# Kernel optimization log

Hardware: AMD Instinct MI355X
Metric: run time of the kernel (lower is better)

The kernel has to match this reference:

```python
import jax, jax.numpy as jnp
import numpy as np

H = 256  # hidden_dim


def _bidir_lstm_layer(x, W_ih, W_hh, bias):
    """x: [S, B, in]; W_ih: [2, in, 4H]; W_hh: [2, H, 4H]; bias: [2, 4H].
    Returns [S, B, 2H] (forward || backward outputs per timestep).
    PyTorch gate order: i, f, g, o."""
    B = x.shape[1]
    init = (jnp.zeros((B, H), x.dtype), jnp.zeros((B, H), x.dtype))
    # precompute input projections for the whole sequence, both directions
    xp = jnp.einsum('sbi,dij->dsbj', x, W_ih) + bias[:, None, None, :]  # [2,S,B,4H]

    def make_step(W_hh_d):
        def step(carry, xt):
            h, c = carry
            g = xt + h @ W_hh_d  # [B, 4H]
            i = jax.nn.sigmoid(g[:, :H])
            f = jax.nn.sigmoid(g[:, H:2 * H])
            gg = jnp.tanh(g[:, 2 * H:3 * H])
            o = jax.nn.sigmoid(g[:, 3 * H:])
            c = f * c + i * gg
            h = o * jnp.tanh(c)
            return (h, c), h
        return step

    _, h_f = jax.lax.scan(make_step(W_hh[0]), init, xp[0])
    _, h_b = jax.lax.scan(make_step(W_hh[1]), init, xp[1], reverse=True)
    return jnp.concatenate([h_f, h_b], axis=-1)  # [S, B, 2H]


def setup_inputs() -> dict:
    key = jax.random.key(0)
    ks = jax.random.split(key, 11)
    s = 0.05  # small init scale to keep gates in their dynamic range
    inp = {
        'x': jax.random.normal(ks[0], (8192, 1024), jnp.float32),
        'w_ih0': jax.random.normal(ks[1], (2, 1024, 4 * H), jnp.float32) * s,
        'w_hh0': jax.random.normal(ks[2], (2, H, 4 * H), jnp.float32) * s,
        'b0': jax.random.normal(ks[3], (2, 4 * H), jnp.float32) * s,
        'w_ih': jax.random.normal(ks[4], (4, 2, 2 * H, 4 * H), jnp.float32) * s,
        'w_hh': jax.random.normal(ks[5], (4, 2, H, 4 * H), jnp.float32) * s,
        'b': jax.random.normal(ks[6], (4, 2, 4 * H), jnp.float32) * s,
        'w1': jax.random.normal(ks[7], (2 * H, 32), jnp.float32) * s,
        'b1': jax.random.normal(ks[8], (32,), jnp.float32) * s,
        'w2': jax.random.normal(ks[9], (32, 2), jnp.float32) * s,
        'b2': jax.random.normal(ks[10], (2,), jnp.float32) * s,
    }
    return inp


def reference(x, w_ih0, w_hh0, b0, w_ih, w_hh, b, w1, b1, w2, b2):
    # x: [S, 1024] -> [S, B=1, 1024] (module does unsqueeze(0).transpose(0,1))
    h = x[:, None, :]
    h = _bidir_lstm_layer(h, w_ih0, w_hh0, b0)
    for l in range(4):  # layers 1..4 (fixed count)
        h = _bidir_lstm_layer(h, w_ih[l], w_hh[l], b[l])
    # cat(forward output at last step, backward output at first step)
    feat = jnp.concatenate([h[-1, :, :H], h[0, :, H:]], axis=1)  # [1, 2H]
    out = (feat @ w1 + b1) @ w2 + b2  # [1, 2]
    return out
```

## Files before the change

kernel.cpp:

```cpp
#include <hip/hip_runtime.h>

constexpr int SQ = 8192;
constexpr int HD = 256;
constexpr int NG = 1024;

typedef __fp16 h2 __attribute__((ext_vector_type(2)));
typedef unsigned int uint;
typedef unsigned short ushort;

__device__ __forceinline__ float sigm_f(float x) {
  float e = __builtin_amdgcn_exp2f(-1.4426950408889634f * x);
  return __builtin_amdgcn_rcpf(1.0f + e);
}
__device__ __forceinline__ float tanh_f(float x) {
  float e = __builtin_amdgcn_exp2f(2.885390081777927f * x);
  return 1.0f - 2.0f * __builtin_amdgcn_rcpf(1.0f + e);
}
__device__ __forceinline__ h2 bch2(uint v) { return __builtin_bit_cast(h2, v); }
__device__ __forceinline__ uint pk(float a, float b) {
  return __builtin_bit_cast(uint, __builtin_amdgcn_cvt_pkrtz(a, b));
}
__device__ __forceinline__ float dpp_xor1(float x) {
  int v = __builtin_amdgcn_mov_dpp(__builtin_bit_cast(int, x), 0xB1, 0xF, 0xF, true);
  return __builtin_bit_cast(float, v);
}

__global__ __launch_bounds__(256) void gemm_xp(const float* __restrict__ A, int K,
                                               const float* __restrict__ W,
                                               const float* __restrict__ bias,
                                               float* __restrict__ out) {
  __shared__ float Al[16][64];
  __shared__ float Bl[16][64];
  const int tid = threadIdx.x;
  const int bm = blockIdx.x * 64;
  const int d  = blockIdx.y >> 4;
  const int bn = (blockIdx.y & 15) * 64;
  const float* Wd = W + (size_t)d * K * NG;
  const float* bd = bias + (size_t)d * NG;
  float* outd = out + (size_t)d * SQ * NG;

  const int m4 = (tid >> 4) << 2;
  const int n4 = (tid & 15) << 2;
  const int am = tid >> 2, ak = (tid & 3) << 2;
  const int bk = tid >> 4, bnn = (tid & 15) << 2;

  float acc[4][4] = {};
  for (int kt = 0; kt < K; kt += 16) {
    float4 av = *(const float4*)(A + (size_t)(bm + am) * K + kt + ak);
    float4 bv = *(const float4*)(Wd + (size_t)(kt + bk) * NG + bn + bnn);
    __syncthreads();
    Al[ak + 0][am] = av.x;
    Al[ak + 1][am] = av.y;
    Al[ak + 2][am] = av.z;
    Al[ak + 3][am] = av.w;
    *(float4*)&Bl[bk][bnn] = bv;
    __syncthreads();
#pragma unroll
    for (int k = 0; k < 16; ++k) {
      float4 a = *(const float4*)&Al[k][m4];
      float4 b = *(const float4*)&Bl[k][n4];
      float ar[4] = {a.x, a.y, a.z, a.w};
      float br[4] = {b.x, b.y, b.z, b.w};
#pragma unroll
      for (int i = 0; i < 4; ++i)
#pragma unroll
        for (int jj = 0; jj < 4; ++jj)
          acc[i][jj] = fmaf(ar[i], br[jj], acc[i][jj]);
    }
  }
#pragma unroll
  for (int i = 0; i < 4; ++i) {
    float4 o;
    o.x = acc[i][0] + bd[bn + n4 + 0];
    o.y = acc[i][1] + bd[bn + n4 + 1];
    o.z = acc[i][2] + bd[bn + n4 + 2];
    o.w = acc[i][3] + bd[bn + n4 + 3];
    *(float4*)(outd + (size_t)(bm + m4 + i) * NG + bn + n4) = o;
  }
}

__global__ __launch_bounds__(512, 1) void lstm_rec11(const float* __restrict__ Whh,
                                                     const float* __restrict__ xp,
                                                     float* __restrict__ obuf) {
  __shared__ uint4 wl[16 * 512];
  __shared__ uint  hl[2][128];
  const int d = blockIdx.x;
  const int j = threadIdx.x;
  const int u = j >> 1;
  const int s = j & 1;
  const float* W   = Whh + (size_t)d * HD * NG;
  const float* xpd = xp + (size_t)d * SQ * NG;

  for (int idx = j; idx < 16 * 512; idx += 512) {
    const int rem = idx & 511;
    const int uu  = rem >> 1;
    const int ss  = rem & 1;
    const int qq  = (idx >> 9) & 3;
    const int g   = idx >> 11;
    const int r0  = ss * 128 + 96 + 8 * qq;
    const int c   = g * 256 + uu;
    uint4 v;
    v.x = pk(W[(size_t)(r0 + 0) * NG + c], W[(size_t)(r0 + 1) * NG + c]);
    v.y = pk(W[(size_t)(r0 + 2) * NG + c], W[(size_t)(r0 + 3) * NG + c]);
    v.z = pk(W[(size_t)(r0 + 4) * NG + c], W[(size_t)(r0 + 5) * NG + c]);
    v.w = pk(W[(size_t)(r0 + 6) * NG + c], W[(size_t)(r0 + 7) * NG + c]);
    wl[idx] = v;
  }

  h2 wr[4][48];
#pragma unroll
  for (int g = 0; g < 4; ++g) {
    const float* Wc = W + (size_t)(s * 128) * NG + g * 256 + u;
#pragma unroll
    for (int k = 0; k < 48; ++k)
      wr[g][k] = __builtin_amdgcn_cvt_pkrtz(Wc[(size_t)(2 * k) * NG],
                                            Wc[(size_t)(2 * k + 1) * NG]);
  }

  if (j < 256) { ((uint*)hl)[j] = 0u; }
  __syncthreads();

  const int fwd = (d == 0) ? 1 : 0;
  int t = fwd ? 0 : SQ - 1;
  const int dt = fwd ? 1 : -1;
  float cc = 0.0f;
  int p = 0;

  float xc[4], xn[4] = {};
#pragma unroll
  for (int g = 0; g < 4; ++g) xc[g] = xpd[(size_t)t * NG + g * 256 + u];

  for (int step = 0; step < SQ; ++step) {
    if (step + 1 < SQ) {
#pragma unroll
      for (int g = 0; g < 4; ++g) xn[g] = xpd[(size_t)(t + dt) * NG + g * 256 + u];
    }

    const uint4* hb = (const uint4*)&hl[p][s * 64];
    float acc[4] = {0.0f, 0.0f, 0.0f, 0.0f};
#pragma unroll
    for (int q = 0; q < 12; ++q) {
      uint4 hq = hb[q];
      h2 hx = bch2(hq.x), hy = bch2(hq.y), hz = bch2(hq.z), hw = bch2(hq.w);
#pragma unroll
      for (int g = 0; g < 4; ++g) {
        acc[g] = __builtin_amdgcn_fdot2(wr[g][4 * q + 0], hx, acc[g], false);
        acc[g] = __builtin_amdgcn_fdot2(wr[g][4 * q + 1], hy, acc[g], false);
        acc[g] = __builtin_amdgcn_fdot2(wr[g][4 * q + 2], hz, acc[g], false);
        acc[g] = __builtin_amdgcn_fdot2(wr[g][4 * q + 3], hw, acc[g], false);
      }
    }
#pragma unroll
    for (int qq = 0; qq < 4; ++qq) {
      uint4 hq = hb[12 + qq];
      h2 hx = bch2(hq.x), hy = bch2(hq.y), hz = bch2(hq.z), hw = bch2(hq.w);
#pragma unroll
      for (int g = 0; g < 4; ++g) {
        uint4 wq = wl[(g * 4 + qq) * 512 + j];
        acc[g] = __builtin_amdgcn_fdot2(bch2(wq.x), hx, acc[g], false);
        acc[g] = __builtin_amdgcn_fdot2(bch2(wq.y), hy, acc[g], false);
        acc[g] = __builtin_amdgcn_fdot2(bch2(wq.z), hz, acc[g], false);
        acc[g] = __builtin_amdgcn_fdot2(bch2(wq.w), hw, acc[g], false);
      }
    }

#pragma unroll
    for (int g = 0; g < 4; ++g) acc[g] += dpp_xor1(acc[g]);

    float iv = sigm_f(acc[0] + xc[0]);
    float fv = sigm_f(acc[1] + xc[1]);
    float gv = tanh_f(acc[2] + xc[2]);
    float ov = sigm_f(acc[3] + xc[3]);
    cc = fv * cc + iv * gv;
    float hv = ov * tanh_f(cc);

    if (s == 0) {
      obuf[(size_t)t * 512 + (d << 8) + u] = hv;
      ((ushort*)hl[p ^ 1])[u] = (ushort)(pk(hv, hv) & 0xFFFFu);
    }

    asm volatile("s_waitcnt lgkmcnt(0)" ::: "memory");
    __builtin_amdgcn_s_barrier();
    __builtin_amdgcn_sched_barrier(0);

    p ^= 1;
#pragma unroll
    for (int g = 0; g < 4; ++g) xc[g] = xn[g];
    t += dt;
  }
}

__global__ void cls_k(const float* __restrict__ buf, const float* __restrict__ w1,
                      const float* __restrict__ b1, const float* __restrict__ w2,
                      const float* __restrict__ b2, float* __restrict__ out) {
  __shared__ float feat[512];
  __shared__ float hid[32];
  const int t = threadIdx.x;
  feat[t] = (t < 256) ? buf[(size_t)(SQ - 1) * 512 + t] : buf[t];
  __syncthreads();
  if (t < 32) {
    float a = b1[t];
    for (int k = 0; k < 512; ++k) a = fmaf(feat[k], w1[k * 32 + t], a);
    hid[t] = a;
  }
  __syncthreads();
  if (t < 2) {
    float a = b2[t];
    for (int k = 0; k < 32; ++k) a = fmaf(hid[k], w2[k * 2 + t], a);
    out[t] = a;
  }
}

extern "C" void kernel_launch(void* const* d_in, const int* in_sizes, int n_in,
                              void* d_out, int out_size, void* d_ws, size_t ws_size,
                              hipStream_t stream) {
  const float* x     = (const float*)d_in[0];
  const float* w_ih0 = (const float*)d_in[1];
  const float* w_hh0 = (const float*)d_in[2];
  const float* b0    = (const float*)d_in[3];
  const float* w_ih  = (const float*)d_in[4];
  const float* w_hh  = (const float*)d_in[5];
  const float* b     = (const float*)d_in[6];
  const float* w1    = (const float*)d_in[7];
  const float* b1    = (const float*)d_in[8];
  const float* w2    = (const float*)d_in[9];
  const float* b2    = (const float*)d_in[10];

  float* xp   = (float*)d_ws;
  float* bufA = xp + (size_t)2 * SQ * NG;
  float* bufB = bufA + (size_t)SQ * 512;

  const dim3 ggrid(SQ / 64, 32);

  gemm_xp<<<ggrid, 256, 0, stream>>>(x, 1024, w_ih0, b0, xp);
  lstm_rec11<<<2, 512, 0, stream>>>(w_hh0, xp, bufA);

  float* cur = bufA;
  float* nxt = bufB;
  for (int lyr = 0; lyr < 4; ++lyr) {
    gemm_xp<<<ggrid, 256, 0, stream>>>(cur, 512, w_ih + (size_t)lyr * 2 * 512 * 1024,
                                       b + (size_t)lyr * 2 * 1024, xp);
    lstm_rec11<<<2, 512, 0, stream>>>(w_hh + (size_t)lyr * 2 * 256 * 1024, xp, nxt);
    float* tmp = cur; cur = nxt; nxt = tmp;
  }

  cls_k<<<1, 512, 0, stream>>>(cur, w1, b1, w2, b2, (float*)d_out);
}
```

Before: 62.86 ms.

## Use split-fp16 MFMA for input projection GEMM and shift more Whh into registers

Replaces the scalar FP32 input-projection GEMM with an MFMA 16x16x32 f16 kernel. Each FP32 operand is split into hi and lo halves, and three MFMAs per tile approximate FP32 precision. The recurrent kernel also moves one more chunk of W_hh rows from LDS into registers (52 instead of 48 packed pairs per gate), cutting per-step LDS weight reads. The risks are more register pressure in the recurrent kernel, reduced accuracy from the split-fp16 scheme, and bank conflicts from the transposed B stores.

```diff
diff --git a/kernel.cpp b/kernel.cpp
--- a/kernel.cpp
+++ b/kernel.cpp
@@ -5,6 +5,8 @@
 constexpr int NG = 1024;
 
 typedef __fp16 h2 __attribute__((ext_vector_type(2)));
+typedef __fp16 f16x8 __attribute__((ext_vector_type(8)));
+typedef float f32x4 __attribute__((ext_vector_type(4)));
 typedef unsigned int uint;
 typedef unsigned short ushort;
 
@@ -20,69 +22,91 @@
 __device__ __forceinline__ uint pk(float a, float b) {
   return __builtin_bit_cast(uint, __builtin_amdgcn_cvt_pkrtz(a, b));
 }
+__device__ __forceinline__ f16x8 bcf(uint4 v) { return __builtin_bit_cast(f16x8, v); }
 __device__ __forceinline__ float dpp_xor1(float x) {
   int v = __builtin_amdgcn_mov_dpp(__builtin_bit_cast(int, x), 0xB1, 0xF, 0xF, true);
   return __builtin_bit_cast(float, v);
 }
 
-__global__ __launch_bounds__(256) void gemm_xp(const float* __restrict__ A, int K,
-                                               const float* __restrict__ W,
-                                               const float* __restrict__ bias,
-                                               float* __restrict__ out) {
-  __shared__ float Al[16][64];
-  __shared__ float Bl[16][64];
+__global__ __launch_bounds__(256) void gemm_mfma(const float* __restrict__ A, int K,
+                                                 const float* __restrict__ W,
+                                                 const float* __restrict__ bias,
+                                                 float* __restrict__ out) {
+  __shared__ __fp16 Ahi[64][40];
+  __shared__ __fp16 Alo[64][40];
+  __shared__ __fp16 Bhi[64][40];
+  __shared__ __fp16 Blo[64][40];
   const int tid = threadIdx.x;
-  const int bm = blockIdx.x * 64;
-  const int d  = blockIdx.y >> 4;
-  const int bn = (blockIdx.y & 15) * 64;
+  const int w   = tid >> 6;
+  const int l   = tid & 63;
+  const int bm  = blockIdx.x * 64;
+  const int d   = blockIdx.y >> 4;
+  const int bn  = (blockIdx.y & 15) * 64;
   const float* Wd = W + (size_t)d * K * NG;
   const float* bd = bias + (size_t)d * NG;
   float* outd = out + (size_t)d * SQ * NG;
 
-  const int m4 = (tid >> 4) << 2;
-  const int n4 = (tid & 15) << 2;
-  const int am = tid >> 2, ak = (tid & 3) << 2;
-  const int bk = tid >> 4, bnn = (tid & 15) << 2;
-
-  float acc[4][4] = {};
-  for (int kt = 0; kt < K; kt += 16) {
-    float4 av = *(const float4*)(A + (size_t)(bm + am) * K + kt + ak);
-    float4 bv = *(const float4*)(Wd + (size_t)(kt + bk) * NG + bn + bnn);
+  const int ar = tid >> 2, ac8 = (tid & 3) * 8;
+  const int br = tid >> 3, bc8 = (tid & 7) * 8;
+
+  f32x4 c[4] = {{0.f, 0.f, 0.f, 0.f}, {0.f, 0.f, 0.f, 0.f},
+                {0.f, 0.f, 0.f, 0.f}, {0.f, 0.f, 0.f, 0.f}};
+
+  for (int kt = 0; kt < K; kt += 32) {
+    float4 a0 = *(const float4*)(A + (size_t)(bm + ar) * K + kt + ac8);
+    float4 a1 = *(const float4*)(A + (size_t)(bm + ar) * K + kt + ac8 + 4);
+    float4 b0 = *(const float4*)(Wd + (size_t)(kt + br) * NG + bn + bc8);
+    float4 b1 = *(const float4*)(Wd + (size_t)(kt + br) * NG + bn + bc8 + 4);
     __syncthreads();
-    Al[ak + 0][am] = av.x;
-    Al[ak + 1][am] = av.y;
-    Al[ak + 2][am] = av.z;
-    Al[ak + 3][am] = av.w;
-    *(float4*)&Bl[bk][bnn] = bv;
+    {
+      float av[8] = {a0.x, a0.y, a0.z, a0.w, a1.x, a1.y, a1.z, a1.w};
+      __fp16 hi[8], lo[8];
+#pragma unroll
+      for (int i = 0; i < 8; ++i) {
+        hi[i] = (__fp16)av[i];
+        lo[i] = (__fp16)(av[i] - (float)hi[i]);
+      }
+      *(uint4*)&Ahi[ar][ac8] = *(const uint4*)hi;
+      *(uint4*)&Alo[ar][ac8] = *(const uint4*)lo;
+    }
+    {
+      float bv[8] = {b0.x, b0.y, b0.z, b0.w, b1.x, b1.y, b1.z, b1.w};
+#pragma unroll
+      for (int i = 0; i < 8; ++i) {
+        __fp16 hi = (__fp16)bv[i];
+        Bhi[bc8 + i][br] = hi;
+        Blo[bc8 + i][br] = (__fp16)(bv[i] - (float)hi);
+      }
+    }
     __syncthreads();
-#pragma unroll
-    for (int k = 0; k < 16; ++k) {
-      float4 a = *(const float4*)&Al[k][m4];
-      float4 b = *(const float4*)&Bl[k][n4];
-      float ar[4] = {a.x, a.y, a.z, a.w};
-      float br[4] = {b.x, b.y, b.z, b.w};
-#pragma unroll
-      for (int i = 0; i < 4; ++i)
-#pragma unroll
-        for (int jj = 0; jj < 4; ++jj)
-          acc[i][jj] = fmaf(ar[i], br[jj], acc[i][jj]);
-    }
-  }
-#pragma unroll
-  for (int i = 0; i < 4; ++i) {
-    float4 o;
-    o.x = acc[i][0] + bd[bn + n4 + 0];
-    o.y = acc[i][1] + bd[bn + n4 + 1];
-    o.z = acc[i][2] + bd[bn + n4 + 2];
-    o.w = acc[i][3] + bd[bn + n4 + 3];
-    *(float4*)(outd + (size_t)(bm + m4 + i) * NG + bn + n4) = o;
-  }
-}
-
-__global__ __launch_bounds__(512, 1) void lstm_rec11(const float* __restrict__ Whh,
+    f16x8 ah = bcf(*(const uint4*)&Ahi[w * 16 + (l & 15)][(l >> 4) * 8]);
+    f16x8 al = bcf(*(const uint4*)&Alo[w * 16 + (l & 15)][(l >> 4) * 8]);
+#pragma unroll
+    for (int nt = 0; nt < 4; ++nt) {
+      f16x8 bh = bcf(*(const uint4*)&Bhi[nt * 16 + (l & 15)][(l >> 4) * 8]);
+      f16x8 bl = bcf(*(const uint4*)&Blo[nt * 16 + (l & 15)][(l >> 4) * 8]);
+      c[nt] = __builtin_amdgcn_mfma_f32_16x16x32_f16(ah, bh, c[nt], 0, 0, 0);
+      c[nt] = __builtin_amdgcn_mfma_f32_16x16x32_f16(al, bh, c[nt], 0, 0, 0);
+      c[nt] = __builtin_amdgcn_mfma_f32_16x16x32_f16(ah, bl, c[nt], 0, 0, 0);
+    }
+  }
+
+#pragma unroll
+  for (int nt = 0; nt < 4; ++nt) {
+    const int col = bn + nt * 16 + (l & 15);
+    const float bb = bd[col];
+#pragma unroll
+    for (int r = 0; r < 4; ++r) {
+      const int row = bm + w * 16 + (l >> 4) * 4 + r;
+      outd[(size_t)row * NG + col] = c[nt][r] + bb;
+    }
+  }
+}
+
+__global__ __launch_bounds__(512, 1) void lstm_rec23(const float* __restrict__ Whh,
                                                      const float* __restrict__ xp,
                                                      float* __restrict__ obuf) {
-  __shared__ uint4 wl[16 * 512];
+  __shared__ uint4 wl[12 * 512];
   __shared__ uint  hl[2][128];
   const int d = blockIdx.x;
   const int j = threadIdx.x;
@@ -91,13 +115,14 @@
   const float* W   = Whh + (size_t)d * HD * NG;
   const float* xpd = xp + (size_t)d * SQ * NG;
 
-  for (int idx = j; idx < 16 * 512; idx += 512) {
+  for (int idx = j; idx < 12 * 512; idx += 512) {
     const int rem = idx & 511;
     const int uu  = rem >> 1;
     const int ss  = rem & 1;
-    const int qq  = (idx >> 9) & 3;
-    const int g   = idx >> 11;
-    const int r0  = ss * 128 + 96 + 8 * qq;
+    const int grp = idx >> 9;
+    const int qq  = grp % 3;
+    const int g   = grp / 3;
+    const int r0  = ss * 128 + 104 + 8 * qq;
     const int c   = g * 256 + uu;
     uint4 v;
     v.x = pk(W[(size_t)(r0 + 0) * NG + c], W[(size_t)(r0 + 1) * NG + c]);
@@ -107,12 +132,12 @@
     wl[idx] = v;
   }
 
-  h2 wr[4][48];
+  h2 wr[4][52];
 #pragma unroll
   for (int g = 0; g < 4; ++g) {
     const float* Wc = W + (size_t)(s * 128) * NG + g * 256 + u;
 #pragma unroll
-    for (int k = 0; k < 48; ++k)
+    for (int k = 0; k < 52; ++k)
       wr[g][k] = __builtin_amdgcn_cvt_pkrtz(Wc[(size_t)(2 * k) * NG],
                                             Wc[(size_t)(2 * k + 1) * NG]);
   }
@@ -139,7 +164,7 @@
     const uint4* hb = (const uint4*)&hl[p][s * 64];
     float acc[4] = {0.0f, 0.0f, 0.0f, 0.0f};
 #pragma unroll
-    for (int q = 0; q < 12; ++q) {
+    for (int q = 0; q < 13; ++q) {
       uint4 hq = hb[q];
       h2 hx = bch2(hq.x), hy = bch2(hq.y), hz = bch2(hq.z), hw = bch2(hq.w);
 #pragma unroll
@@ -151,12 +176,12 @@
       }
     }
 #pragma unroll
-    for (int qq = 0; qq < 4; ++qq) {
-      uint4 hq = hb[12 + qq];
+    for (int qq = 0; qq < 3; ++qq) {
+      uint4 hq = hb[13 + qq];
       h2 hx = bch2(hq.x), hy = bch2(hq.y), hz = bch2(hq.z), hw = bch2(hq.w);
 #pragma unroll
       for (int g = 0; g < 4; ++g) {
-        uint4 wq = wl[(g * 4 + qq) * 512 + j];
+        uint4 wq = wl[(g * 3 + qq) * 512 + j];
         acc[g] = __builtin_amdgcn_fdot2(bch2(wq.x), hx, acc[g], false);
         acc[g] = __builtin_amdgcn_fdot2(bch2(wq.y), hy, acc[g], false);
         acc[g] = __builtin_amdgcn_fdot2(bch2(wq.z), hz, acc[g], false);
@@ -232,15 +257,15 @@
 
   const dim3 ggrid(SQ / 64, 32);
 
-  gemm_xp<<<ggrid, 256, 0, stream>>>(x, 1024, w_ih0, b0, xp);
-  lstm_rec11<<<2, 512, 0, stream>>>(w_hh0, xp, bufA);
+  gemm_mfma<<<ggrid, 256, 0, stream>>>(x, 1024, w_ih0, b0, xp);
+  lstm_rec23<<<2, 512, 0, stream>>>(w_hh0, xp, bufA);
 
   float* cur = bufA;
   float* nxt = bufB;
   for (int lyr = 0; lyr < 4; ++lyr) {
-    gemm_xp<<<ggrid, 256, 0, stream>>>(cur, 512, w_ih + (size_t)lyr * 2 * 512 * 1024,
-                                       b + (size_t)lyr * 2 * 1024, xp);
-    lstm_rec11<<<2, 512, 0, stream>>>(w_hh + (size_t)lyr * 2 * 256 * 1024, xp, nxt);
+    gemm_mfma<<<ggrid, 256, 0, stream>>>(cur, 512, w_ih + (size_t)lyr * 2 * 512 * 1024,
+                                         b + (size_t)lyr * 2 * 1024, xp);
+    lstm_rec23<<<2, 512, 0, stream>>>(w_hh + (size_t)lyr * 2 * 256 * 1024, xp, nxt);
     float* tmp = cur; cur = nxt; nxt = tmp;
   }
 
```

After: 69.02 ms. 9.8% more time.
